# Kernel optimization log

Hardware: AMD Instinct MI355X
Metric: run time of the kernel (lower is better)

## Reference

```python
import jax, jax.numpy as jnp
import numpy as np

N = 100000        # nodes (== node_num)
E = 3200000       # edges
C = 8             # hidden (sparse=False branch)
HEADS = 2
GROUPS = 8
LAYERS = 3
FEAT = 16
EMB = 8
NCLS = 2


def glin(x, W, b):
    # PyG grouped Linear: x [..., C], W [G, C//G, C//G], b [C]
    G, cin, cout = W.shape
    xg = x.reshape(*x.shape[:-1], G, cin)
    out = jnp.einsum('...gi,gio->...go', xg, W)
    return out.reshape(*x.shape[:-1], G * cout) + b


def gcn_norm(edge_index, num_nodes):
    # symmetric GCN normalization with added self-loops, unit edge weights
    loop = jnp.arange(num_nodes, dtype=edge_index.dtype)
    src = jnp.concatenate([edge_index[0], loop])
    dst = jnp.concatenate([edge_index[1], loop])
    w = jnp.ones(src.shape[0], dtype=jnp.float32)
    deg = jax.ops.segment_sum(w, dst, num_segments=num_nodes)
    dinv = jnp.where(deg > 0, jax.lax.rsqrt(deg), 0.0)
    return src, dst, dinv[src] * dinv[dst]


def dna_conv(x_all, src, dst, norm, Wq, bq, Wk, bk, Wv, bv):
    # PyG DNAConv (eval mode): target's latest history entry attends over the
    # source neighbor's full history. x_all: [N, L, C].
    n, L, c = x_all.shape
    d = c // HEADS
    # q/k/v linears are per-entry -> compute per node, gather per edge (same math)
    q = glin(x_all[:, -1], Wq, bq).reshape(n, HEADS, d)    # [N,H,d]
    k = glin(x_all, Wk, bk).reshape(n, L, HEADS, d)        # [N,L,H,d]
    v = glin(x_all, Wv, bv).reshape(n, L, HEADS, d)
    qe = q[dst]                                            # [E',H,d]
    score = jnp.einsum('ehd,elhd->ehl', qe, k[src]) * (1.0 / np.sqrt(d))
    attn = jax.nn.softmax(score, axis=-1)                  # softmax over history L
    out = jnp.einsum('ehl,elhd->ehd', attn, v[src]).reshape(-1, c)
    out = out * norm[:, None]
    return jax.ops.segment_sum(out, dst, num_segments=n)   # aggr='add' at target


def setup_inputs():
    ks = jax.random.split(jax.random.key(0), 16)
    s = 0.5
    return {
        'x': jax.random.normal(ks[0], (N, FEAT), dtype=jnp.float32),
        'node_index': jnp.arange(N),
        'node_one_hot': jnp.zeros((N,), dtype=jnp.int32),
        'edge_index': jax.random.randint(ks[1], (2, E), 0, N),
        'edge_weight': jax.random.uniform(ks[2], (E,), dtype=jnp.float32),
        'emb_table': jax.random.normal(ks[3], (N, EMB), dtype=jnp.float32) * 0.1,
        'W1': jax.random.normal(ks[4], (EMB + FEAT, C), dtype=jnp.float32) * 0.2,
        'b1': jnp.zeros((C,), dtype=jnp.float32),
        'Wq': jax.random.normal(ks[5], (LAYERS, GROUPS, C // GROUPS, C // GROUPS), dtype=jnp.float32) * s,
        'bq': jnp.zeros((LAYERS, C), dtype=jnp.float32),
        'Wk': jax.random.normal(ks[6], (LAYERS, GROUPS, C // GROUPS, C // GROUPS), dtype=jnp.float32) * s,
        'bk': jnp.zeros((LAYERS, C), dtype=jnp.float32),
        'Wv': jax.random.normal(ks[7], (LAYERS, GROUPS, C // GROUPS, C // GROUPS), dtype=jnp.float32) * s,
        'bv': jnp.zeros((LAYERS, C), dtype=jnp.float32),
        'W2': jax.random.normal(ks[8], (C, NCLS), dtype=jnp.float32) * 0.3,
        'b2': jnp.zeros((NCLS,), dtype=jnp.float32),
    }


def reference(x, node_index, node_one_hot, edge_index, edge_weight,
              emb_table, W1, b1, Wq, bq, Wk, bk, Wv, bv, W2, b2):
    # node_one_hot / edge_weight are unpacked but unused in the original forward
    h = jnp.concatenate([emb_table[node_index], x], axis=1)   # [N, EMB+FEAT]
    h = jax.nn.relu(h @ W1 + b1)                              # [N, C]
    x_all = h[:, None, :]                                     # history [N, 1, C]
    src, dst, norm = gcn_norm(edge_index, x.shape[0])
    for i in range(LAYERS):
        h = jax.nn.relu(dna_conv(x_all, src, dst, norm,
                                 Wq[i], bq[i], Wk[i], bk[i], Wv[i], bv[i]))
        x_all = jnp.concatenate([x_all, h[:, None, :]], axis=1)
    logits = x_all[:, -1] @ W2 + b2
    return jax.nn.log_softmax(logits, axis=-1)
```

## Files before the change

kernel.cpp:

```cpp
#include <hip/hip_runtime.h>
#include <math.h>


#define SBB   8
#define SBN   256
#define CH    4096
#define CAP   9216

typedef _Float16 half8 __attribute__((ext_vector_type(8)));
typedef int int4v __attribute__((ext_vector_type(4)));

__global__ void __launch_bounds__(256) phaseAC(const int* __restrict__ eidx,
                                               int* __restrict__ gcnt,
                                               int* __restrict__ ebuf,
                                               int E, int NS) {
    __shared__ int sorted_[CH];
    __shared__ unsigned short karr[CH];
    __shared__ int cntS[512];
    __shared__ int lofs[512];
    __shared__ int wbase[512];
    __shared__ int sA[512], sB[512];
    int t = threadIdx.x, b = blockIdx.x;
    int base = b * CH;
    int nEdge = E - base; if (nEdge > CH) nEdge = CH;

    for (int i = t; i < 512; i += 256) cntS[i] = 0;
    __syncthreads();

    int w[16]; short kk[16];
#pragma unroll
    for (int it = 0; it < 4; it++) {
        int e0 = base + (it * 256 + t) * 4;
        if (e0 + 3 < E) {
            int4v s4 = __builtin_nontemporal_load((const int4v*)(eidx + e0));
            int4v d4 = __builtin_nontemporal_load((const int4v*)(eidx + E + e0));
#pragma unroll
            for (int j = 0; j < 4; j++) {
                int idx = it * 4 + j;
                w[idx] = s4[j] | ((d4[j] & (SBN - 1)) << 17);
                kk[idx] = (short)(d4[j] >> SBB);
                atomicAdd(&cntS[kk[idx]], 1);
            }
        } else {
#pragma unroll
            for (int j = 0; j < 4; j++) {
                int e = e0 + j, idx = it * 4 + j;
                if (e < E) {
                    int s = eidx[e], d = eidx[E + e];
                    w[idx] = s | ((d & (SBN - 1)) << 17);
                    kk[idx] = (short)(d >> SBB);
                    atomicAdd(&cntS[kk[idx]], 1);
                } else { w[idx] = 0; kk[idx] = 511; }
            }
        }
    }
    __syncthreads();
    sA[t] = cntS[t]; sA[t + 256] = cntS[t + 256];
    __syncthreads();
    int* sp = sA; int* dp = sB;
    for (int o = 1; o < 512; o <<= 1) {
#pragma unroll
        for (int h = 0; h < 2; h++) {
            int i = t + h * 256;
            int v = sp[i];
            if (i >= o) v += sp[i - o];
            dp[i] = v;
        }
        __syncthreads();
        int* tmp = sp; sp = dp; dp = tmp;
    }
    for (int i = t; i < 512; i += 256) {
        int excl = sp[i] - cntS[i];
        lofs[i] = excl;
        if (i < NS && cntS[i] > 0) {
            int g = atomicAdd(&gcnt[i], cntS[i]);
            wbase[i] = i * CAP + g - excl;
        }
    }
    __syncthreads();
#pragma unroll
    for (int idx = 0; idx < 16; idx++) {
        if (kk[idx] != 511) {
            int p = atomicAdd(&lofs[kk[idx]], 1);
            sorted_[p] = w[idx];
            karr[p] = (unsigned short)kk[idx];
        }
    }
    __syncthreads();
    for (int i = t; i < nEdge; i += 256)
        ebuf[wbase[karr[i]] + i] = sorted_[i];
}

__global__ void super_csr(int* __restrict__ ebuf, const int* __restrict__ gcnt,
                          unsigned int* __restrict__ off, char* __restrict__ A,
                          char* __restrict__ U, int NS, int n) {
    __shared__ int seg[CAP];
    __shared__ int cnt[SBN];
    __shared__ int fillp[SBN];
    __shared__ int sd[256];
    int t = threadIdx.x, k = blockIdx.x;
    cnt[t] = 0;
    int start = k * CAP;
    int len = gcnt[k];
    __syncthreads();
    for (int i = t; i < len; i += 256) {
        int w = __builtin_nontemporal_load(&ebuf[start + i]);
        seg[i] = w;
        atomicAdd(&cnt[w >> 17], 1);
    }
    __syncthreads();
    int v = cnt[t];
    sd[t] = v; __syncthreads();
    for (int o = 1; o < 256; o <<= 1) {
        int u = 0; if (t >= o) u = sd[t - o];
        __syncthreads(); sd[t] += u; __syncthreads();
    }
    int excl = sd[t] - v;
    fillp[t] = excl;
    int d = (k << SBB) + t;
    if (d < n) {
        off[d] = (unsigned int)(start + excl) | ((unsigned int)v << 22);
        float dvv = rsqrtf((float)(v + 1));
        *(float*)(A + (size_t)d * 32 + 16) = dvv;
        *(float*)(U + (size_t)d * 64 + 48) = dvv;
    }
    __syncthreads();
    for (int i = t; i < len; i += 256) {
        int w = seg[i];
        int pos = atomicAdd(&fillp[w >> 17], 1);
        ebuf[start + pos] = w & 131071;
    }
}

__global__ void node_init(const float* __restrict__ x, const int* __restrict__ nidx,
                          const float* __restrict__ emb, const float* __restrict__ W1,
                          const float* __restrict__ b1, char* __restrict__ A,
                          char* __restrict__ U, int* __restrict__ gcnt,
                          int NS, int n) {
    int i = blockIdx.x * blockDim.x + threadIdx.x;
    if (i < NS) gcnt[i] = 0;
    if (i >= n) return;
    float in[24];
    int ni = nidx[i];
    const float4* ep = (const float4*)(emb + (size_t)ni * 8);
    float4 e0 = ep[0], e1 = ep[1];
    in[0] = e0.x; in[1] = e0.y; in[2] = e0.z; in[3] = e0.w;
    in[4] = e1.x; in[5] = e1.y; in[6] = e1.z; in[7] = e1.w;
    const float4* xp = (const float4*)(x + (size_t)i * 16);
#pragma unroll
    for (int t = 0; t < 4; t++) {
        float4 v = xp[t];
        in[8 + 4 * t + 0] = v.x; in[8 + 4 * t + 1] = v.y;
        in[8 + 4 * t + 2] = v.z; in[8 + 4 * t + 3] = v.w;
    }
    float acc[8];
#pragma unroll
    for (int j = 0; j < 8; j++) acc[j] = b1[j];
#pragma unroll
    for (int t = 0; t < 24; t++) {
        float xv = in[t];
#pragma unroll
        for (int j = 0; j < 8; j++) acc[j] = fmaf(xv, W1[t * 8 + j], acc[j]);
    }
    half8 h;
#pragma unroll
    for (int j = 0; j < 8; j++) h[j] = (_Float16)fmaxf(acc[j], 0.0f);
    *(half8*)(A + (size_t)i * 32) = h;
    *(half8*)(U + (size_t)i * 64) = h;
}

template <int Li, bool LAST>
__global__ void __launch_bounds__(256)
agg_layer(int* __restrict__ ssrc, const unsigned int* __restrict__ off,
          const char* __restrict__ A, char* __restrict__ U,
          const float* __restrict__ wq, const float* __restrict__ bq,
          const float* __restrict__ wk, const float* __restrict__ bk,
          const float* __restrict__ wv, const float* __restrict__ bv,
          const float* __restrict__ W2, const float* __restrict__ b2,
          float* __restrict__ out, int n) {
    constexpr int B = (Li == 1) ? 8 : 4;
    int tid = blockIdx.x * blockDim.x + threadIdx.x;
    int d = tid >> 3, t = tid & 7;
    if (d >= n) return;
    unsigned int ow = off[d];
    int lo = (int)(ow & 0x3FFFFFu), cnt = (int)(ow >> 22);

    float nd, SN;
    if (Li == 1) {
        nd = *(const float*)(A + (size_t)d * 32 + 16);
        SN = 0.f;
    } else {
        float2 nn = *(const float2*)(U + (size_t)d * 64 + 48);
        nd = nn.x; SN = nn.y;
    }

    float qk[8];
    if (Li >= 2) {
        half8 qh = (Li == 2) ? *(const half8*)(U + (size_t)d * 64 + 16)
                             : *(const half8*)(U + (size_t)d * 64 + 32);
#pragma unroll
        for (int c = 0; c < 8; c++) {
            float qv = fmaf((float)qh[c], wq[c], bq[c]);
            qk[c] = 0.72134752f * wk[c] * qv;
        }
    }

    float T[8];
#pragma unroll
    for (int c = 0; c < 8; c++) T[c] = 0.f;

    int total = cnt + 1;

    for (int s0 = t; s0 < total; s0 += 8 * B) {
        int m = (total - s0 + 7) >> 3; if (m > B) m = B;
        unsigned int w[B]; int si[B]; float ns[B];
        half8 r[B][Li];
#pragma unroll
        for (int u = 0; u < B; u++) {
            int s = s0 + 8 * u;
            w[u] = 0u;
            if (u < m && s > 0)
                w[u] = (unsigned int)__builtin_nontemporal_load(ssrc + lo + s - 1);
        }
#pragma unroll
        for (int u = 0; u < B; u++) {
            if (u < m) {
                int s = s0 + 8 * u;
                si[u] = (s == 0) ? d : (int)(w[u] & 0x1FFFFu);
                if (Li == 1) {
                    const char* p = A + (size_t)si[u] * 32;
                    r[u][0] = *(const half8*)p;
                    ns[u] = (s == 0) ? nd : *(const float*)(p + 16);
                } else {
                    const char* p = U + (size_t)si[u] * 64;
#pragma unroll
                    for (int l = 0; l < Li; l++) r[u][l] = *(const half8*)(p + l * 16);
                    ns[u] = (s == 0) ? nd : (float)(w[u] >> 17) * (1.0f / 32767.0f);
                }
            }
        }
#pragma unroll
        for (int u = 0; u < B; u++) {
            if (u < m) {
                float xs[8 * Li];
#pragma unroll
                for (int l = 0; l < Li; l++)
#pragma unroll
                    for (int c = 0; c < 8; c++) xs[l * 8 + c] = (float)r[u][l][c];
                float nv = ns[u];
                if (Li == 1) {
#pragma unroll
                    for (int c = 0; c < 8; c++) T[c] = fmaf(nv, xs[c], T[c]);
                    SN += nv;
                } else {
                    float score[2][Li];
#pragma unroll
                    for (int l = 0; l < Li; l++) {
#pragma unroll
                        for (int h = 0; h < 2; h++) {
                            float sc = 0.f;
#pragma unroll
                            for (int dd = 0; dd < 4; dd++) {
                                int c = h * 4 + dd;
                                sc = fmaf(qk[c], xs[l * 8 + c], sc);
                            }
                            score[h][l] = sc;
                        }
                    }
                    float f[2][Li];
#pragma unroll
                    for (int h = 0; h < 2; h++) {
                        float ssum = 0.f;
#pragma unroll
                        for (int l = 0; l < Li; l++) { f[h][l] = exp2f(score[h][l]); ssum += f[h][l]; }
                        float nsh = nv * __builtin_amdgcn_rcpf(ssum);
#pragma unroll
                        for (int l = 0; l < Li; l++) f[h][l] *= nsh;
                    }
#pragma unroll
                    for (int c = 0; c < 8; c++) {
                        int h = c >> 2;
#pragma unroll
                        for (int l = 0; l < Li; l++) T[c] = fmaf(f[h][l], xs[l * 8 + c], T[c]);
                    }
                }
            }
        }
        if (Li == 1) {
#pragma unroll
            for (int u = 0; u < B; u++) {
                int s = s0 + 8 * u;
                if (u < m && s > 0) {
                    unsigned int q = (unsigned int)(ns[u] * 32767.0f + 0.5f);
                    int packed = (int)(w[u] | (q << 17));
                    __builtin_nontemporal_store(packed, ssrc + lo + s - 1);
                }
            }
        }
    }
#pragma unroll
    for (int m2 = 1; m2 < 8; m2 <<= 1) {
#pragma unroll
        for (int c = 0; c < 8; c++) T[c] += __shfl_xor(T[c], m2);
        if (Li == 1) SN += __shfl_xor(SN, m2);
    }
    if (!LAST) {
        float acc = fmaf(wv[t], T[t], bv[t] * SN);
        float h = fmaxf(acc * nd, 0.f);
        *(_Float16*)(U + (size_t)d * 64 + Li * 16 + 2 * t) = (_Float16)h;
        if (Li == 1 && t == 1)
            *(float*)(U + (size_t)d * 64 + 52) = SN;
    } else if (t == 0) {
        float z0 = b2[0], z1 = b2[1];
#pragma unroll
        for (int c = 0; c < 8; c++) {
            float acc = fmaf(wv[c], T[c], bv[c] * SN);
            float h = fmaxf(acc * nd, 0.f);
            z0 = fmaf(h, W2[c * 2 + 0], z0);
            z1 = fmaf(h, W2[c * 2 + 1], z1);
        }
        float m2 = fmaxf(z0, z1);
        float lse = m2 + logf(__expf(z0 - m2) + __expf(z1 - m2));
        ((float2*)out)[d] = make_float2(z0 - lse, z1 - lse);
    }
}

extern "C" void kernel_launch(void* const* d_in, const int* in_sizes, int n_in,
                              void* d_out, int out_size, void* d_ws, size_t ws_size,
                              hipStream_t stream) {
    const float* x    = (const float*)d_in[0];
    const int*   nidx = (const int*)d_in[1];
    const int*   eidx = (const int*)d_in[3];
    const float* emb  = (const float*)d_in[5];
    const float* W1   = (const float*)d_in[6];
    const float* b1   = (const float*)d_in[7];
    const float* Wq   = (const float*)d_in[8];
    const float* bq   = (const float*)d_in[9];
    const float* Wk   = (const float*)d_in[10];
    const float* bk   = (const float*)d_in[11];
    const float* Wv   = (const float*)d_in[12];
    const float* bv   = (const float*)d_in[13];
    const float* W2   = (const float*)d_in[14];
    const float* b2   = (const float*)d_in[15];
    float* out = (float*)d_out;

    const int n = in_sizes[0] / 16;
    const int E = in_sizes[3] / 2;
    const int NS = (n + SBN - 1) / SBN;
    const int NBLK = (E + CH - 1) / CH;

    char* wsp = (char*)d_ws;
    char*  A     = wsp;                      wsp += (size_t)n * 32;
    char*  U     = wsp;                      wsp += (size_t)n * 64;
    int*   ebuf  = (int*)wsp;                wsp += (size_t)NS * CAP * 4;
    unsigned int* off = (unsigned int*)wsp;  wsp += (size_t)n * 4;
    int*   gcnt  = (int*)wsp;                wsp += (size_t)NS * 4;

    dim3 blk(256);
    dim3 gn((n + 255) / 256);
    dim3 ga(((size_t)n * 8 + 255) / 256);

    node_init<<<gn, blk, 0, stream>>>(x, nidx, emb, W1, b1, A, U, gcnt, NS, n);
    phaseAC<<<NBLK, blk, 0, stream>>>(eidx, gcnt, ebuf, E, NS);
    super_csr<<<NS, blk, 0, stream>>>(ebuf, gcnt, off, A, U, NS, n);

    agg_layer<1, false><<<ga, blk, 0, stream>>>(ebuf, off, A, U,
        Wq, bq, Wk, bk, Wv, bv, W2, b2, out, n);
    agg_layer<2, false><<<ga, blk, 0, stream>>>(ebuf, off, A, U,
        Wq + 8, bq + 8, Wk + 8, bk + 8, Wv + 8, bv + 8, W2, b2, out, n);
    agg_layer<3, true><<<ga, blk, 0, stream>>>(ebuf, off, A, U,
        Wq + 16, bq + 16, Wk + 16, bk + 16, Wv + 16, bv + 16, W2, b2, out, n);
}
```

Baseline: 273.8 us.

## Pad per-node edge lists to multiples of eight with dummy zero node

Result: slower. 295.7 us (+8.0%).

```diff
diff --git a/kernel.cpp b/kernel.cpp
--- a/kernel.cpp
+++ b/kernel.cpp
@@ -5,7 +5,7 @@
 #define SBB   8
 #define SBN   256
 #define CH    4096
-#define CAP   9216
+#define CAP   10240
 
 typedef _Float16 half8 __attribute__((ext_vector_type(8)));
 typedef int int4v __attribute__((ext_vector_type(4)));
@@ -110,16 +110,17 @@
     }
     __syncthreads();
     int v = cnt[t];
-    sd[t] = v; __syncthreads();
+    int p = ((v + 8) & ~7) - 1;
+    sd[t] = p; __syncthreads();
     for (int o = 1; o < 256; o <<= 1) {
         int u = 0; if (t >= o) u = sd[t - o];
         __syncthreads(); sd[t] += u; __syncthreads();
     }
-    int excl = sd[t] - v;
-    fillp[t] = excl;
+    int exclp = sd[t] - p;
+    fillp[t] = exclp;
     int d = (k << SBB) + t;
     if (d < n) {
-        off[d] = (unsigned int)(start + excl) | ((unsigned int)v << 22);
+        off[d] = (unsigned int)(start + exclp) | ((unsigned int)p << 22);
         float dvv = rsqrtf((float)(v + 1));
         *(float*)(A + (size_t)d * 32 + 16) = dvv;
         *(float*)(U + (size_t)d * 64 + 48) = dvv;
@@ -129,6 +130,10 @@
         int w = seg[i];
         int pos = atomicAdd(&fillp[w >> 17], 1);
         ebuf[start + pos] = w & 131071;
+    }
+    if (d < n) {
+        for (int i = v; i < p; i++)
+            ebuf[start + exclp + i] = n;
     }
 }
 
@@ -139,6 +144,13 @@
                           int NS, int n) {
     int i = blockIdx.x * blockDim.x + threadIdx.x;
     if (i < NS) gcnt[i] = 0;
+    if (i == n) {
+        float4 z = make_float4(0.f, 0.f, 0.f, 0.f);
+        float4* ap = (float4*)(A + (size_t)n * 32);
+        ap[0] = z; ap[1] = z;
+        float4* up = (float4*)(U + (size_t)n * 64);
+        up[0] = z; up[1] = z; up[2] = z; up[3] = z;
+    }
     if (i >= n) return;
     float in[24];
     int ni = nidx[i];
@@ -178,7 +190,7 @@
           const float* __restrict__ wv, const float* __restrict__ bv,
           const float* __restrict__ W2, const float* __restrict__ b2,
           float* __restrict__ out, int n) {
-    constexpr int B = (Li == 1) ? 8 : 4;
+    constexpr int B = (Li == 1) ? 8 : 5;
     int tid = blockIdx.x * blockDim.x + threadIdx.x;
     int d = tid >> 3, t = tid & 7;
     if (d >= n) return;
@@ -209,15 +221,15 @@
 #pragma unroll
     for (int c = 0; c < 8; c++) T[c] = 0.f;
 
-    int total = cnt + 1;
-
-    for (int s0 = t; s0 < total; s0 += 8 * B) {
-        int m = (total - s0 + 7) >> 3; if (m > B) m = B;
+    int R = (cnt + 1) >> 3;
+
+    for (int r0 = 0; r0 < R; r0 += B) {
+        int m = R - r0; if (m > B) m = B;
         unsigned int w[B]; int si[B]; float ns[B];
         half8 r[B][Li];
 #pragma unroll
         for (int u = 0; u < B; u++) {
-            int s = s0 + 8 * u;
+            int s = (r0 + u) * 8 + t;
             w[u] = 0u;
             if (u < m && s > 0)
                 w[u] = (unsigned int)__builtin_nontemporal_load(ssrc + lo + s - 1);
@@ -225,7 +237,7 @@
 #pragma unroll
         for (int u = 0; u < B; u++) {
             if (u < m) {
-                int s = s0 + 8 * u;
+                int s = (r0 + u) * 8 + t;
                 si[u] = (s == 0) ? d : (int)(w[u] & 0x1FFFFu);
                 if (Li == 1) {
                     const char* p = A + (size_t)si[u] * 32;
@@ -289,7 +301,7 @@
         if (Li == 1) {
 #pragma unroll
             for (int u = 0; u < B; u++) {
-                int s = s0 + 8 * u;
+                int s = (r0 + u) * 8 + t;
                 if (u < m && s > 0) {
                     unsigned int q = (unsigned int)(ns[u] * 32767.0f + 0.5f);
                     int packed = (int)(w[u] | (q << 17));
@@ -350,14 +362,14 @@
     const int NBLK = (E + CH - 1) / CH;
 
     char* wsp = (char*)d_ws;
-    char*  A     = wsp;                      wsp += (size_t)n * 32;
-    char*  U     = wsp;                      wsp += (size_t)n * 64;
+    char*  A     = wsp;                      wsp += (size_t)(n + 1) * 32;
+    char*  U     = wsp;                      wsp += (size_t)(n + 1) * 64;
     int*   ebuf  = (int*)wsp;                wsp += (size_t)NS * CAP * 4;
     unsigned int* off = (unsigned int*)wsp;  wsp += (size_t)n * 4;
     int*   gcnt  = (int*)wsp;                wsp += (size_t)NS * 4;
 
     dim3 blk(256);
-    dim3 gn((n + 255) / 256);
+    dim3 gn((n + 1 + 255) / 256);
     dim3 ga(((size_t)n * 8 + 255) / 256);
 
     node_init<<<gn, blk, 0, stream>>>(x, nidx, emb, W1, b1, A, U, gcnt, NS, n);
```
